# Kernel tuning notes

Hardware: AMD Instinct MI355X
Metric: run time of the kernel (lower is better)

## Reference

```python
import jax, jax.numpy as jnp
import numpy as np

L, D, V, F4 = 12, 768, 50304, 3072
B, T = 4, 1024


def setup_inputs() -> dict:
    key = jax.random.key(0)
    ks = jax.random.split(key, 12)
    s = 0.02
    return {
        "idx": jax.random.randint(ks[0], (B, T), 0, V),
        "targets": jax.random.randint(ks[1], (B, T), 0, V),
        "wte": jax.random.normal(ks[2], (V, D), jnp.float32) * s,  # tied with lm_head
        "pos_embed": jax.random.normal(ks[3], (L, D), jnp.float32),  # per-block (1,1,D) learned pos embed
        "dyt_alpha": jnp.full((L, 3), 0.5, jnp.float32),  # dyt, dyt2, dyt3 alphas
        "dyt_w": jnp.ones((L, 3, D), jnp.float32),
        "dyt_b": jnp.zeros((L, 3, D), jnp.float32),
        "Wq": jax.random.normal(ks[4], (L, D, D), jnp.float32) * s,
        "Wk": jax.random.normal(ks[5], (L, D, D), jnp.float32) * s,
        "Wv": jax.random.normal(ks[6], (L, D, D), jnp.float32) * s,
        "Wp": jax.random.normal(ks[7], (L, D, D), jnp.float32) * s,
        "bp": jnp.zeros((L, D), jnp.float32),
        "We": jax.random.normal(ks[8], (L, F4, D), jnp.float32) * s,
        "be": jnp.zeros((L, F4), jnp.float32),
        "Wc": jax.random.normal(ks[9], (L, D, F4), jnp.float32) * s,
        "bc": jnp.zeros((L, D), jnp.float32),
    }


def _dyt(x, a, w, b):
    return jnp.tanh(a * x) * w + b


def _forward(idx, targets, wte, pos_embed, dyt_alpha, dyt_w, dyt_b,
             Wq, Wk, Wv, Wp, bp, We, be, Wc, bc):
    b, t = idx.shape
    x = wte[idx]  # (b,t,D)
    pos = jnp.arange(t)
    pbias = -jnp.abs(pos[None, :] - pos[:, None]).astype(x.dtype)  # (t,t) ALiBi-style bias
    scale = 1.0 / np.sqrt(D)  # note: source scales by sqrt(emb_dim), not head dim
    total_kl = jnp.asarray(0.0, x.dtype)
    for l in range(L):
        xl = x + pos_embed[l][None, None, :]
        prior = _dyt(xl, dyt_alpha[l, 2], dyt_w[l, 2], dyt_b[l, 2])  # dyt3
        h = _dyt(xl, dyt_alpha[l, 0], dyt_w[l, 0], dyt_b[l, 0])      # dyt (dropout=0)
        Q = jnp.einsum('btd,od->bto', h, Wq[l])
        K = jnp.einsum('btd,od->bto', h, Wk[l])
        Vv = jnp.einsum('btd,od->bto', h, Wv[l])
        scores = jnp.einsum('btd,bsd->bts', Q, K) * scale + pbias  # (b,t,t), no causal mask
        aw = jax.nn.softmax(scores, axis=-1)
        ao = jnp.einsum('bts,bsd->btd', aw, Vv)
        ao = jnp.einsum('btd,od->bto', ao, Wp[l]) + bp[l]
        h2 = _dyt(ao, dyt_alpha[l, 1], dyt_w[l, 1], dyt_b[l, 1])     # dyt2
        h2 = jax.nn.gelu(jnp.einsum('btd,fd->btf', h2, We[l]) + be[l], approximate=False)
        h2 = jnp.einsum('btf,df->btd', h2, Wc[l]) + bc[l]
        posterior = h2 + prior
        m = 0.5 * (prior + posterior)
        lm = jax.nn.log_softmax(m, axis=-1)
        mp = jnp.exp(lm)
        lp = jax.nn.log_softmax(prior, axis=-1)
        lq = jax.nn.log_softmax(posterior, axis=-1)
        # F.kl_div(log_p, q, reduction='batchmean') = sum(q*(log q - log_p)) / batch
        kl = 0.5 * (jnp.sum(mp * (lm - lp)) + jnp.sum(mp * (lm - lq))) / b
        total_kl = total_kl + kl
        x = posterior
    logits = jnp.einsum('btd,vd->btv', x[:, -1:, :], wte)  # (b,1,V)
    full_logits = jnp.einsum('btd,vd->btv', x, wte)
    lsm = jax.nn.log_softmax(full_logits, axis=-1)
    nll = -jnp.take_along_axis(lsm, targets[..., None], axis=-1).squeeze(-1)
    loss = jnp.mean(nll) + total_kl * 0.1
    return logits, loss


def reference(idx, targets, wte, pos_embed, dyt_alpha, dyt_w, dyt_b,
              Wq, Wk, Wv, Wp, bp, We, be, Wc, bc):
    return _forward(idx, targets, wte, pos_embed, dyt_alpha, dyt_w, dyt_b,
                    Wq, Wk, Wv, Wp, bp, We, be, Wc, bc)
```

## Files before the change

### kernel.cpp

```cpp
#include <hip/hip_runtime.h>
#include <hip/hip_bf16.h>

typedef __attribute__((ext_vector_type(8))) short bf16x8;
typedef __attribute__((ext_vector_type(4))) float f32x4;

__device__ __forceinline__ short f2bf(float f) {
  unsigned u = __float_as_uint(f);
  u = u + 0x7fffu + ((u >> 16) & 1u);
  return (short)(u >> 16);
}
__device__ __forceinline__ float bf2f(short s) {
  return __uint_as_float(((unsigned)(unsigned short)s) << 16);
}

#define GLOB_CAST(p) ((const __attribute__((address_space(1))) void*)(p))
#define LDS_CAST(p) ((__attribute__((address_space(3))) void*)(p))
#define GLL16(g, l) __builtin_amdgcn_global_load_lds(GLOB_CAST(g), LDS_CAST(l), 16, 0, 0)

constexpr int EP_BF16 = 0, EP_SCORES = 1, EP_DYT = 2, EP_GELU = 3, EP_PRIOR = 4;

__global__ __launch_bounds__(256) void cvt_k(const float* __restrict__ src,
                                             short* __restrict__ dst, long n4) {
  const long s = (long)blockIdx.x * 256 + threadIdx.x;
  if (s >= n4) return;
  float4 v = ((const float4*)src)[s];
  short4 o = {f2bf(v.x), f2bf(v.y), f2bf(v.z), f2bf(v.w)};
  ((short4*)dst)[s] = o;
}

__global__ __launch_bounds__(256) void cvt_layer_k(
    const float* __restrict__ wq, const float* __restrict__ wk,
    const float* __restrict__ wv, const float* __restrict__ wp,
    const float* __restrict__ we, const float* __restrict__ wc,
    short* __restrict__ dst) {
  const long s = (long)blockIdx.x * 256 + threadIdx.x;
  const long e = s * 4;
  const float* src; long off;
  if (e < 589824)        { src = wq; off = e; }
  else if (e < 1179648)  { src = wk; off = e - 589824; }
  else if (e < 1769472)  { src = wv; off = e - 1179648; }
  else if (e < 2359296)  { src = wp; off = e - 1769472; }
  else if (e < 4718592)  { src = we; off = e - 2359296; }
  else                   { src = wc; off = e - 4718592; }
  float4 v = *(const float4*)(src + off);
  short4 o = {f2bf(v.x), f2bf(v.y), f2bf(v.z), f2bf(v.w)};
  *(short4*)(dst + e) = o;
}

__global__ __launch_bounds__(256) void embed_head_k(
    const int* __restrict__ idx, const float* __restrict__ wte,
    const float* __restrict__ pos, const float* __restrict__ alp,
    const float* __restrict__ w, const float* __restrict__ b,
    float* __restrict__ x, float* __restrict__ prior, short* __restrict__ h) {
  const long s = (long)blockIdx.x * 256 + threadIdx.x;
  const long row = s / 192;
  const int c4 = (int)(s % 192);
  float4 xv = ((const float4*)(wte + (long)idx[row] * 768))[c4];
  ((float4*)x)[s] = xv;
  float4 pv = ((const float4*)pos)[c4];
  float4 w0 = ((const float4*)w)[c4];
  float4 b0 = ((const float4*)b)[c4];
  float4 w2 = ((const float4*)(w + 1536))[c4];
  float4 b2 = ((const float4*)(b + 1536))[c4];
  const float a0 = alp[0], a2 = alp[2];
  float4 xl = {xv.x + pv.x, xv.y + pv.y, xv.z + pv.z, xv.w + pv.w};
  float4 pr = {tanhf(a2 * xl.x) * w2.x + b2.x, tanhf(a2 * xl.y) * w2.y + b2.y,
               tanhf(a2 * xl.z) * w2.z + b2.z, tanhf(a2 * xl.w) * w2.w + b2.w};
  ((float4*)prior)[s] = pr;
  short4 hh = {f2bf(tanhf(a0 * xl.x) * w0.x + b0.x),
               f2bf(tanhf(a0 * xl.y) * w0.y + b0.y),
               f2bf(tanhf(a0 * xl.z) * w0.z + b0.z),
               f2bf(tanhf(a0 * xl.w) * w0.w + b0.w)};
  ((short4*)h)[s] = hh;
}

template <int EP, int TN>
__global__ __launch_bounds__(256, 2) void gemm_bt(
    const short* __restrict__ A, const short* __restrict__ B,
    void* __restrict__ Cv, int K, int lda, int ldb, int ldc,
    long sA, long sB, long sC,
    const float* __restrict__ bias, const float* __restrict__ dw,
    const float* __restrict__ db, const float* __restrict__ alp,
    const float* __restrict__ prior, float scale) {
  constexpr int NF = TN / 32;
  __shared__ short As[128 * 64];
  __shared__ short Bs[TN * 64];
  const int tid = threadIdx.x, lane = tid & 63;
  const int wr = tid >> 7, wc = (tid >> 6) & 1;
  const long rowBase = (long)blockIdx.y * 128;
  const long colBase = (long)blockIdx.x * TN;
  const short* Ab = A + (long)blockIdx.z * sA;
  const short* Bb = B + (long)blockIdx.z * sB;
  const int srow = tid >> 3, sseg = tid & 7;
  const int ssegS = sseg ^ (srow & 7);

  f32x4 acc[4][NF];
#pragma unroll
  for (int m = 0; m < 4; ++m)
#pragma unroll
    for (int n = 0; n < NF; ++n) acc[m][n] = (f32x4){0.f, 0.f, 0.f, 0.f};

  const int q = lane >> 4, cl = lane & 15;
  const int rsw = cl & 7;

  for (int kt = 0; kt < K; kt += 64) {
#pragma unroll
    for (int i = 0; i < 4; ++i)
      GLL16(Ab + (rowBase + i * 32 + srow) * (long)lda + kt + ssegS * 8,
            As + ((i * 32 + srow) * 64 + sseg * 8));
#pragma unroll
    for (int i = 0; i < TN / 32; ++i)
      GLL16(Bb + (colBase + i * 32 + srow) * (long)ldb + kt + ssegS * 8,
            Bs + ((i * 32 + srow) * 64 + sseg * 8));
    __syncthreads();
#pragma unroll
    for (int kk = 0; kk < 2; ++kk) {
      const int sw = ((kk * 4 + q) ^ rsw) << 3;
      bf16x8 af[4], bfr[NF];
#pragma unroll
      for (int m = 0; m < 4; ++m)
        af[m] = *(const bf16x8*)&As[(wr * 64 + m * 16 + cl) * 64 + sw];
#pragma unroll
      for (int n = 0; n < NF; ++n)
        bfr[n] = *(const bf16x8*)&Bs[(wc * (TN / 2) + n * 16 + cl) * 64 + sw];
#pragma unroll
      for (int m = 0; m < 4; ++m)
#pragma unroll
        for (int n = 0; n < NF; ++n)
          acc[m][n] = __builtin_amdgcn_mfma_f32_16x16x32_bf16(af[m], bfr[n], acc[m][n], 0, 0, 0);
    }
    __syncthreads();
  }

#pragma unroll
  for (int m = 0; m < 4; ++m) {
#pragma unroll
    for (int n = 0; n < NF; ++n) {
#pragma unroll
      for (int j = 0; j < 4; ++j) {
        long r = rowBase + wr * 64 + m * 16 + q * 4 + j;
        long c = colBase + wc * (TN / 2) + n * 16 + cl;
        float v = acc[m][n][j];
        if constexpr (EP == EP_SCORES) {
          float pb = -fabsf((float)(int)(r - c));
          ((float*)Cv)[(long)blockIdx.z * sC + r * ldc + c] = v * scale + pb;
        } else if constexpr (EP == EP_BF16) {
          ((short*)Cv)[(long)blockIdx.z * sC + r * ldc + c] = f2bf(v);
        } else if constexpr (EP == EP_DYT) {
          float xv = v + bias[c];
          ((short*)Cv)[r * (long)ldc + c] = f2bf(tanhf(alp[0] * xv) * dw[c] + db[c]);
        } else if constexpr (EP == EP_GELU) {
          float xv = v + bias[c];
          ((short*)Cv)[r * (long)ldc + c] = f2bf(0.5f * xv * (1.f + erff(xv * 0.70710678118654752f)));
        } else if constexpr (EP == EP_PRIOR) {
          ((float*)Cv)[r * (long)ldc + c] = v + bias[c] + prior[r * (long)ldc + c];
        }
      }
    }
  }
}

__global__ __launch_bounds__(256) void transp_k(const short* __restrict__ V,
                                                short* __restrict__ Vt, int ldv) {
  __shared__ short t[32][33];
  const int b = blockIdx.z;
  const int d0 = blockIdx.x * 32, t0 = blockIdx.y * 32;
  const int tx = threadIdx.x & 31, ty = threadIdx.x >> 5;
  const short* Vb = V + (long)b * 1024 * ldv;
  short* Tb = Vt + (long)b * 768 * 1024;
#pragma unroll
  for (int i = 0; i < 4; ++i)
    t[ty + i * 8][tx] = Vb[(long)(t0 + ty + i * 8) * ldv + d0 + tx];
  __syncthreads();
#pragma unroll
  for (int i = 0; i < 4; ++i)
    Tb[(long)(d0 + ty + i * 8) * 1024 + t0 + tx] = t[tx][ty + i * 8];
}

__global__ __launch_bounds__(256) void softmax_k(float* __restrict__ sc) {
  const int lane = threadIdx.x & 63;
  const long row = (long)blockIdx.x * 4 + (threadIdx.x >> 6);
  const float4* p = (const float4*)(sc + row * 1024);
  float4 v[4];
  float mx = -3e38f;
#pragma unroll
  for (int i = 0; i < 4; ++i) {
    v[i] = p[lane * 4 + i];
    mx = fmaxf(mx, fmaxf(fmaxf(v[i].x, v[i].y), fmaxf(v[i].z, v[i].w)));
  }
#pragma unroll
  for (int o = 1; o < 64; o <<= 1) mx = fmaxf(mx, __shfl_xor(mx, o));
  float e[16];
  float s = 0.f;
#pragma unroll
  for (int i = 0; i < 4; ++i) {
    e[i * 4 + 0] = __expf(v[i].x - mx);
    e[i * 4 + 1] = __expf(v[i].y - mx);
    e[i * 4 + 2] = __expf(v[i].z - mx);
    e[i * 4 + 3] = __expf(v[i].w - mx);
    s += e[i * 4] + e[i * 4 + 1] + e[i * 4 + 2] + e[i * 4 + 3];
  }
#pragma unroll
  for (int o = 1; o < 64; o <<= 1) s += __shfl_xor(s, o);
  const float inv = 1.f / s;
  short4* dst = (short4*)((short*)sc + row * 2048);
#pragma unroll
  for (int i = 0; i < 4; ++i) {
    short4 o4 = {f2bf(e[i * 4] * inv), f2bf(e[i * 4 + 1] * inv),
                 f2bf(e[i * 4 + 2] * inv), f2bf(e[i * 4 + 3] * inv)};
    dst[lane * 4 + i] = o4;
  }
}

__global__ __launch_bounds__(256) void tail_k(
    float* __restrict__ prior, const float* __restrict__ post,
    const float* __restrict__ pos_n, const float* __restrict__ alp_n,
    const float* __restrict__ w_n, const float* __restrict__ b_n,
    short* __restrict__ h, short* __restrict__ xbf,
    double* __restrict__ acc, int last) {
  const int lane = threadIdx.x & 63;
  const long row = (long)blockIdx.x * 4 + (threadIdx.x >> 6);
  float* pp = prior + row * 768;
  const float* qq = post + row * 768;
  float p[12], q[12];
#pragma unroll
  for (int i = 0; i < 12; ++i) { p[i] = pp[lane + i * 64]; q[i] = qq[lane + i * 64]; }
  float mp = -3e38f, mq = -3e38f, mm = -3e38f;
#pragma unroll
  for (int i = 0; i < 12; ++i) {
    float m = 0.5f * (p[i] + q[i]);
    mp = fmaxf(mp, p[i]); mq = fmaxf(mq, q[i]); mm = fmaxf(mm, m);
  }
#pragma unroll
  for (int o = 1; o < 64; o <<= 1) {
    mp = fmaxf(mp, __shfl_xor(mp, o));
    mq = fmaxf(mq, __shfl_xor(mq, o));
    mm = fmaxf(mm, __shfl_xor(mm, o));
  }
  float sp = 0.f, sq = 0.f, sm = 0.f;
#pragma unroll
  for (int i = 0; i < 12; ++i) {
    sp += __expf(p[i] - mp);
    sq += __expf(q[i] - mq);
    sm += __expf(0.5f * (p[i] + q[i]) - mm);
  }
#pragma unroll
  for (int o = 1; o < 64; o <<= 1) {
    sp += __shfl_xor(sp, o); sq += __shfl_xor(sq, o); sm += __shfl_xor(sm, o);
  }
  const float lseP = mp + logf(sp), lseQ = mq + logf(sq), lseM = mm + logf(sm);
  float kl = 0.f;
#pragma unroll
  for (int i = 0; i < 12; ++i) {
    float m = 0.5f * (p[i] + q[i]);
    float lm = m - lseM;
    kl += __expf(lm) * (2.f * lm - (p[i] - lseP) - (q[i] - lseQ));
  }
#pragma unroll
  for (int o = 1; o < 64; o <<= 1) kl += __shfl_xor(kl, o);
  if (lane == 0) atomicAdd(&acc[0], (double)kl);

  if (last) {
#pragma unroll
    for (int i = 0; i < 12; ++i) xbf[row * 768 + lane + i * 64] = f2bf(q[i]);
  } else {
    const float a0 = alp_n[0], a2 = alp_n[2];
#pragma unroll
    for (int i = 0; i < 12; ++i) {
      const int col = lane + i * 64;
      float xl = q[i] + pos_n[col];
      pp[col] = tanhf(a2 * xl) * w_n[1536 + col] + b_n[1536 + col];
      h[row * 768 + col] = f2bf(tanhf(a0 * xl) * w_n[col] + b_n[col]);
    }
  }
}

__global__ __launch_bounds__(256, 2) void lse_gemm_k(
    const short* __restrict__ Xb, const short* __restrict__ Wt,
    float* __restrict__ pm, float* __restrict__ ps,
    float* __restrict__ logits_out, int G) {
  __shared__ short As[128 * 64];
  __shared__ short Bs[128 * 64];
  __shared__ float pmx[2][128], psm[2][128], rm[128], rs[128];
  const int tid = threadIdx.x, lane = tid & 63;
  const int wr = tid >> 7, wc = (tid >> 6) & 1;
  const int g = blockIdx.x;
  const long rowBase = (long)blockIdx.y * 128;
  const int srow = tid >> 3, sseg = tid & 7;
  const int ssegS = sseg ^ (srow & 7);
  const int q = lane >> 4, cl = lane & 15;
  const int rsw = cl & 7;
  if (tid < 128) { rm[tid] = -3e38f; rs[tid] = 0.f; }

  for (int tile = g; tile < 393; tile += G) {
    const long colBase = (long)tile * 128;
    f32x4 acc[4][4];
#pragma unroll
    for (int m = 0; m < 4; ++m)
#pragma unroll
      for (int n = 0; n < 4; ++n) acc[m][n] = (f32x4){0.f, 0.f, 0.f, 0.f};

    for (int kt = 0; kt < 768; kt += 64) {
#pragma unroll
      for (int i = 0; i < 4; ++i) {
        GLL16(Xb + (rowBase + i * 32 + srow) * 768L + kt + ssegS * 8,
              As + ((i * 32 + srow) * 64 + sseg * 8));
        GLL16(Wt + (colBase + i * 32 + srow) * 768L + kt + ssegS * 8,
              Bs + ((i * 32 + srow) * 64 + sseg * 8));
      }
      __syncthreads();
#pragma unroll
      for (int kk = 0; kk < 2; ++kk) {
        const int sw = ((kk * 4 + q) ^ rsw) << 3;
        bf16x8 af[4], bfr[4];
#pragma unroll
        for (int m = 0; m < 4; ++m)
          af[m] = *(const bf16x8*)&As[(wr * 64 + m * 16 + cl) * 64 + sw];
#pragma unroll
        for (int n = 0; n < 4; ++n)
          bfr[n] = *(const bf16x8*)&Bs[(wc * 64 + n * 16 + cl) * 64 + sw];
#pragma unroll
        for (int m = 0; m < 4; ++m)
#pragma unroll
          for (int n = 0; n < 4; ++n)
            acc[m][n] = __builtin_amdgcn_mfma_f32_16x16x32_bf16(af[m], bfr[n], acc[m][n], 0, 0, 0);
      }
      __syncthreads();
    }

#pragma unroll
    for (int m = 0; m < 4; ++m)
#pragma unroll
      for (int n = 0; n < 4; ++n)
#pragma unroll
        for (int j = 0; j < 4; ++j) {
          long r = rowBase + wr * 64 + m * 16 + q * 4 + j;
          if ((r & 1023) == 1023) {
            long c = colBase + wc * 64 + n * 16 + cl;
            logits_out[(r >> 10) * 50304 + c] = acc[m][n][j];
          }
        }

#pragma unroll
    for (int m = 0; m < 4; ++m) {
#pragma unroll
      for (int j = 0; j < 4; ++j) {
        float mx = acc[m][0][j];
#pragma unroll
        for (int n = 1; n < 4; ++n) mx = fmaxf(mx, acc[m][n][j]);
#pragma unroll
        for (int o = 1; o < 16; o <<= 1) mx = fmaxf(mx, __shfl_xor(mx, o));
        float sm = 0.f;
#pragma unroll
        for (int n = 0; n < 4; ++n) sm += __expf(acc[m][n][j] - mx);
#pragma unroll
        for (int o = 1; o < 16; o <<= 1) sm += __shfl_xor(sm, o);
        if (cl == 0) {
          int lr = wr * 64 + m * 16 + q * 4 + j;
          pmx[wc][lr] = mx;
          psm[wc][lr] = sm;
        }
      }
    }
    __syncthreads();
    if (tid < 128) {
      float m0 = pmx[0][tid], m1 = pmx[1][tid];
      float m2 = fmaxf(m0, m1);
      float s2 = psm[0][tid] * __expf(m0 - m2) + psm[1][tid] * __expf(m1 - m2);
      float mo = rm[tid], mn = fmaxf(mo, m2);
      rs[tid] = rs[tid] * __expf(mo - mn) + s2 * __expf(m2 - mn);
      rm[tid] = mn;
    }
    __syncthreads();
  }
  if (tid < 128) {
    long row = rowBase + tid;
    pm[row * G + g] = rm[tid];
    ps[row * G + g] = rs[tid];
  }
}

__global__ __launch_bounds__(256) void tlog_k(const short* __restrict__ xbf,
                                              const short* __restrict__ wtebf,
                                              const int* __restrict__ targets,
                                              float* __restrict__ tlog) {
  const int lane = threadIdx.x & 63;
  const long row = (long)blockIdx.x * 4 + (threadIdx.x >> 6);
  const long tgt = targets[row];
  const short* a = xbf + row * 768;
  const short* b = wtebf + tgt * 768;
  float s = 0.f;
#pragma unroll
  for (int i = 0; i < 12; ++i) s += bf2f(a[lane + i * 64]) * bf2f(b[lane + i * 64]);
#pragma unroll
  for (int o = 1; o < 64; o <<= 1) s += __shfl_xor(s, o);
  if (lane == 0) tlog[row] = s;
}

__global__ __launch_bounds__(256) void stage2_k(const float* __restrict__ pm,
                                                const float* __restrict__ ps,
                                                const float* __restrict__ tlog,
                                                double* __restrict__ acc, int G) {
  const long row = (long)blockIdx.x * 256 + threadIdx.x;
  float M = -3e38f;
  for (int gi = 0; gi < G; ++gi) M = fmaxf(M, pm[row * G + gi]);
  float S = 0.f;
  for (int gi = 0; gi < G; ++gi) S += ps[row * G + gi] * __expf(pm[row * G + gi] - M);
  float nll = (M + logf(S)) - tlog[row];
#pragma unroll
  for (int o = 1; o < 64; o <<= 1) nll += __shfl_xor(nll, o);
  if ((threadIdx.x & 63) == 0) atomicAdd(&acc[1], (double)nll);
}

__global__ void finalize_k(const double* __restrict__ acc, float* __restrict__ out) {
  if (threadIdx.x == 0)
    out[201216] = (float)(acc[1] / 4096.0 + 0.1 * 0.5 * acc[0] / 4.0);
}

constexpr size_t OFF_WTEBF = 0;
constexpr size_t OFF_LW    = 77266944;
constexpr size_t OFF_X     = 91422720;
constexpr size_t OFF_PRIOR = 104005632;
constexpr size_t OFF_HB    = 116588544;
constexpr size_t OFF_U1    = 122880000;
constexpr size_t OFF_QKV   = OFF_U1;
constexpr size_t OFF_VT    = OFF_U1 + 18874368;
constexpr size_t OFF_E     = OFF_U1;
constexpr size_t OFF_SC    = 148045824;
constexpr size_t OFF_AO    = 164823040;
constexpr size_t OFF_XBF   = 171114496;
constexpr size_t OFF_PM    = 177405952;
constexpr size_t OFF_PS    = 177799168;
constexpr size_t OFF_TLOG  = 178192384;
constexpr size_t OFF_ACC   = 178208768;
constexpr size_t WS_NEED   = 178208784;

extern "C" void kernel_launch(void* const* d_in, const int* in_sizes, int n_in,
                              void* d_out, int out_size, void* d_ws, size_t ws_size,
                              hipStream_t stream) {
  const int* idx = (const int*)d_in[0];
  const int* targets = (const int*)d_in[1];
  const float* wte = (const float*)d_in[2];
  const float* pos = (const float*)d_in[3];
  const float* dalpha = (const float*)d_in[4];
  const float* dytw = (const float*)d_in[5];
  const float* dytb = (const float*)d_in[6];
  const float* Wq = (const float*)d_in[7];
  const float* Wk = (const float*)d_in[8];
  const float* Wv = (const float*)d_in[9];
  const float* Wp = (const float*)d_in[10];
  const float* bp = (const float*)d_in[11];
  const float* We = (const float*)d_in[12];
  const float* be = (const float*)d_in[13];
  const float* Wc = (const float*)d_in[14];
  const float* bc = (const float*)d_in[15];
  float* out = (float*)d_out;

  if (ws_size < WS_NEED) return;
  char* ws = (char*)d_ws;
  short* WTEBF = (short*)(ws + OFF_WTEBF);
  short* LW = (short*)(ws + OFF_LW);
  float* X = (float*)(ws + OFF_X);
  float* PRIOR = (float*)(ws + OFF_PRIOR);
  short* HB = (short*)(ws + OFF_HB);
  short* QKVB = (short*)(ws + OFF_QKV);
  short* VT = (short*)(ws + OFF_VT);
  short* E = (short*)(ws + OFF_E);
  float* SC = (float*)(ws + OFF_SC);
  short* AW = (short*)(ws + OFF_SC);
  short* AO = (short*)(ws + OFF_AO);
  short* XBF = (short*)(ws + OFF_XBF);
  float* PM = (float*)(ws + OFF_PM);
  float* PS = (float*)(ws + OFF_PS);
  float* TLOG = (float*)(ws + OFF_TLOG);
  double* ACC = (double*)(ws + OFF_ACC);

  hipMemsetAsync(ACC, 0, 16, stream);
  cvt_k<<<37728, 256, 0, stream>>>(wte, WTEBF, 9658368);
  embed_head_k<<<3072, 256, 0, stream>>>(idx, wte, pos, dalpha, dytw, dytb, X, PRIOR, HB);

  const float scale = 0.03608439182435161f;

  for (int l = 0; l < 12; ++l) {
    cvt_layer_k<<<6912, 256, 0, stream>>>(Wq + (long)l * 589824, Wk + (long)l * 589824,
                                          Wv + (long)l * 589824, Wp + (long)l * 589824,
                                          We + (long)l * 2359296, Wc + (long)l * 2359296, LW);
    gemm_bt<EP_BF16, 128><<<dim3(18, 32, 1), 256, 0, stream>>>(
        HB, LW, QKVB, 768, 768, 768, 2304, 0, 0, 0,
        nullptr, nullptr, nullptr, nullptr, nullptr, 0.f);
    transp_k<<<dim3(24, 32, 4), 256, 0, stream>>>(QKVB + 1536, VT, 2304);
    gemm_bt<EP_SCORES, 64><<<dim3(16, 8, 4), 256, 0, stream>>>(
        QKVB, QKVB + 768, SC, 768, 2304, 2304, 1024,
        2359296, 2359296, 1048576, nullptr, nullptr, nullptr, nullptr, nullptr, scale);
    softmax_k<<<1024, 256, 0, stream>>>(SC);
    gemm_bt<EP_BF16, 64><<<dim3(12, 8, 4), 256, 0, stream>>>(
        AW, VT, AO, 1024, 2048, 1024, 768, 2097152, 786432, 786432,
        nullptr, nullptr, nullptr, nullptr, nullptr, 0.f);
    gemm_bt<EP_DYT, 64><<<dim3(12, 32, 1), 256, 0, stream>>>(
        AO, LW + 1769472, HB, 768, 768, 768, 768, 0, 0, 0,
        bp + l * 768, dytw + l * 2304 + 768, dytb + l * 2304 + 768,
        dalpha + l * 3 + 1, nullptr, 0.f);
    gemm_bt<EP_GELU, 128><<<dim3(24, 32, 1), 256, 0, stream>>>(
        HB, LW + 2359296, E, 768, 768, 768, 3072, 0, 0, 0,
        be + l * 3072, nullptr, nullptr, nullptr, nullptr, 0.f);
    gemm_bt<EP_PRIOR, 64><<<dim3(12, 32, 1), 256, 0, stream>>>(
        E, LW + 4718592, X, 3072, 3072, 3072, 768, 0, 0, 0,
        bc + l * 768, nullptr, nullptr, nullptr, PRIOR, 0.f);
    tail_k<<<1024, 256, 0, stream>>>(PRIOR, X, pos + (l + 1) * 768,
                                     dalpha + (l + 1) * 3, dytw + (l + 1) * 2304,
                                     dytb + (l + 1) * 2304, HB, XBF, ACC, l == 11);
  }

  lse_gemm_k<<<dim3(24, 32), 256, 0, stream>>>(XBF, WTEBF, PM, PS, out, 24);
  tlog_k<<<1024, 256, 0, stream>>>(XBF, WTEBF, targets, TLOG);
  stage2_k<<<16, 256, 0, stream>>>(PM, PS, TLOG, ACC, 24);
  finalize_k<<<1, 64, 0, stream>>>(ACC, out);
}
```

Baseline: 3.111 ms.

## Fuse V transpose into QKV GEMM, batch weight conversion, add BK template

The QKV GEMM gains an epilogue that writes V directly in transposed layout, which removes the separate transpose kernel. When the workspace is large enough, all layer weights are converted to bf16 in one kernel up front instead of once per layer. The GEMM also gets a K-tile template parameter, set to 128 for the narrow-N GEMMs so they need fewer sync iterations, at the cost of more LDS per block. The transposed V stores are uncoalesced and the big path depends on the workspace size the harness provides.

```diff
diff --git a/kernel.cpp b/kernel.cpp
--- a/kernel.cpp
+++ b/kernel.cpp
@@ -17,7 +17,7 @@
 #define LDS_CAST(p) ((__attribute__((address_space(3))) void*)(p))
 #define GLL16(g, l) __builtin_amdgcn_global_load_lds(GLOB_CAST(g), LDS_CAST(l), 16, 0, 0)
 
-constexpr int EP_BF16 = 0, EP_SCORES = 1, EP_DYT = 2, EP_GELU = 3, EP_PRIOR = 4;
+constexpr int EP_BF16 = 0, EP_SCORES = 1, EP_DYT = 2, EP_GELU = 3, EP_PRIOR = 4, EP_QKVT = 5;
 
 __global__ __launch_bounds__(256) void cvt_k(const float* __restrict__ src,
                                              short* __restrict__ dst, long n4) {
@@ -45,6 +45,27 @@
   float4 v = *(const float4*)(src + off);
   short4 o = {f2bf(v.x), f2bf(v.y), f2bf(v.z), f2bf(v.w)};
   *(short4*)(dst + e) = o;
+}
+
+__global__ __launch_bounds__(256) void cvt_all_k(
+    const float* __restrict__ wq, const float* __restrict__ wk,
+    const float* __restrict__ wv, const float* __restrict__ wp,
+    const float* __restrict__ we, const float* __restrict__ wc,
+    short* __restrict__ dst) {
+  const long s = (long)blockIdx.x * 256 + threadIdx.x;
+  if (s >= 21233664L) return;
+  const long l = s / 1769472;
+  const long e = (s - l * 1769472) * 4;
+  const float* src; long off;
+  if (e < 589824)        { src = wq + l * 589824;  off = e; }
+  else if (e < 1179648)  { src = wk + l * 589824;  off = e - 589824; }
+  else if (e < 1769472)  { src = wv + l * 589824;  off = e - 1179648; }
+  else if (e < 2359296)  { src = wp + l * 589824;  off = e - 1769472; }
+  else if (e < 4718592)  { src = we + l * 2359296; off = e - 2359296; }
+  else                   { src = wc + l * 2359296; off = e - 4718592; }
+  float4 v = *(const float4*)(src + off);
+  short4 o = {f2bf(v.x), f2bf(v.y), f2bf(v.z), f2bf(v.w)};
+  *(short4*)(dst + l * 7077888 + e) = o;
 }
 
 __global__ __launch_bounds__(256) void embed_head_k(
@@ -74,24 +95,27 @@
   ((short4*)h)[s] = hh;
 }
 
-template <int EP, int TN>
+template <int EP, int TN, int BK>
 __global__ __launch_bounds__(256, 2) void gemm_bt(
     const short* __restrict__ A, const short* __restrict__ B,
-    void* __restrict__ Cv, int K, int lda, int ldb, int ldc,
+    void* __restrict__ Cv, short* __restrict__ vt,
+    int K, int lda, int ldb, int ldc,
     long sA, long sB, long sC,
     const float* __restrict__ bias, const float* __restrict__ dw,
     const float* __restrict__ db, const float* __restrict__ alp,
     const float* __restrict__ prior, float scale) {
   constexpr int NF = TN / 32;
-  __shared__ short As[128 * 64];
-  __shared__ short Bs[TN * 64];
+  constexpr int SEGS = BK / 8;
+  constexpr int RPR = 2048 / BK;
+  __shared__ short As[128 * BK];
+  __shared__ short Bs[TN * BK];
   const int tid = threadIdx.x, lane = tid & 63;
   const int wr = tid >> 7, wc = (tid >> 6) & 1;
   const long rowBase = (long)blockIdx.y * 128;
   const long colBase = (long)blockIdx.x * TN;
   const short* Ab = A + (long)blockIdx.z * sA;
   const short* Bb = B + (long)blockIdx.z * sB;
-  const int srow = tid >> 3, sseg = tid & 7;
+  const int srow = tid / SEGS, sseg = tid % SEGS;
   const int ssegS = sseg ^ (srow & 7);
 
   f32x4 acc[4][NF];
@@ -103,26 +127,30 @@
   const int q = lane >> 4, cl = lane & 15;
   const int rsw = cl & 7;
 
-  for (int kt = 0; kt < K; kt += 64) {
-#pragma unroll
-    for (int i = 0; i < 4; ++i)
-      GLL16(Ab + (rowBase + i * 32 + srow) * (long)lda + kt + ssegS * 8,
-            As + ((i * 32 + srow) * 64 + sseg * 8));
-#pragma unroll
-    for (int i = 0; i < TN / 32; ++i)
-      GLL16(Bb + (colBase + i * 32 + srow) * (long)ldb + kt + ssegS * 8,
-            Bs + ((i * 32 + srow) * 64 + sseg * 8));
+  for (int kt = 0; kt < K; kt += BK) {
+#pragma unroll
+    for (int i = 0; i < BK / 16; ++i) {
+      const int row = i * RPR + srow;
+      GLL16(Ab + (rowBase + row) * (long)lda + kt + ssegS * 8,
+            As + (row * BK + sseg * 8));
+    }
+#pragma unroll
+    for (int i = 0; i < TN * BK / 2048; ++i) {
+      const int row = i * RPR + srow;
+      GLL16(Bb + (colBase + row) * (long)ldb + kt + ssegS * 8,
+            Bs + (row * BK + sseg * 8));
+    }
     __syncthreads();
 #pragma unroll
-    for (int kk = 0; kk < 2; ++kk) {
+    for (int kk = 0; kk < BK / 32; ++kk) {
       const int sw = ((kk * 4 + q) ^ rsw) << 3;
       bf16x8 af[4], bfr[NF];
 #pragma unroll
       for (int m = 0; m < 4; ++m)
-        af[m] = *(const bf16x8*)&As[(wr * 64 + m * 16 + cl) * 64 + sw];
+        af[m] = *(const bf16x8*)&As[(wr * 64 + m * 16 + cl) * BK + sw];
 #pragma unroll
       for (int n = 0; n < NF; ++n)
-        bfr[n] = *(const bf16x8*)&Bs[(wc * (TN / 2) + n * 16 + cl) * 64 + sw];
+        bfr[n] = *(const bf16x8*)&Bs[(wc * (TN / 2) + n * 16 + cl) * BK + sw];
 #pragma unroll
       for (int m = 0; m < 4; ++m)
 #pragma unroll
@@ -146,6 +174,11 @@
           ((float*)Cv)[(long)blockIdx.z * sC + r * ldc + c] = v * scale + pb;
         } else if constexpr (EP == EP_BF16) {
           ((short*)Cv)[(long)blockIdx.z * sC + r * ldc + c] = f2bf(v);
+        } else if constexpr (EP == EP_QKVT) {
+          if (c < 1536)
+            ((short*)Cv)[r * (long)ldc + c] = f2bf(v);
+          else
+            vt[(r >> 10) * 786432 + (c - 1536) * 1024 + (r & 1023)] = f2bf(v);
         } else if constexpr (EP == EP_DYT) {
           float xv = v + bias[c];
           ((short*)Cv)[r * (long)ldc + c] = f2bf(tanhf(alp[0] * xv) * dw[c] + db[c]);
@@ -158,23 +191,6 @@
       }
     }
   }
-}
-
-__global__ __launch_bounds__(256) void transp_k(const short* __restrict__ V,
-                                                short* __restrict__ Vt, int ldv) {
-  __shared__ short t[32][33];
-  const int b = blockIdx.z;
-  const int d0 = blockIdx.x * 32, t0 = blockIdx.y * 32;
-  const int tx = threadIdx.x & 31, ty = threadIdx.x >> 5;
-  const short* Vb = V + (long)b * 1024 * ldv;
-  short* Tb = Vt + (long)b * 768 * 1024;
-#pragma unroll
-  for (int i = 0; i < 4; ++i)
-    t[ty + i * 8][tx] = Vb[(long)(t0 + ty + i * 8) * ldv + d0 + tx];
-  __syncthreads();
-#pragma unroll
-  for (int i = 0; i < 4; ++i)
-    Tb[(long)(d0 + ty + i * 8) * 1024 + t0 + tx] = t[tx][ty + i * 8];
 }
 
 __global__ __launch_bounds__(256) void softmax_k(float* __restrict__ sc) {
@@ -433,7 +449,9 @@
 constexpr size_t OFF_PS    = 177799168;
 constexpr size_t OFF_TLOG  = 178192384;
 constexpr size_t OFF_ACC   = 178208768;
-constexpr size_t WS_NEED   = 178208784;
+constexpr size_t WS_SMALL  = 178208784;
+constexpr size_t OFF_LWALL = 178208784;
+constexpr size_t WS_BIG    = 348078096;
 
 extern "C" void kernel_launch(void* const* d_in, const int* in_sizes, int n_in,
                               void* d_out, int out_size, void* d_ws, size_t ws_size,
@@ -456,10 +474,12 @@
   const float* bc = (const float*)d_in[15];
   float* out = (float*)d_out;
 
-  if (ws_size < WS_NEED) return;
+  if (ws_size < WS_SMALL) return;
+  const bool big = ws_size >= WS_BIG;
   char* ws = (char*)d_ws;
   short* WTEBF = (short*)(ws + OFF_WTEBF);
   short* LW = (short*)(ws + OFF_LW);
+  short* LWALL = (short*)(ws + OFF_LWALL);
   float* X = (float*)(ws + OFF_X);
   float* PRIOR = (float*)(ws + OFF_PRIOR);
   short* HB = (short*)(ws + OFF_HB);
@@ -477,34 +497,41 @@
 
   hipMemsetAsync(ACC, 0, 16, stream);
   cvt_k<<<37728, 256, 0, stream>>>(wte, WTEBF, 9658368);
+  if (big)
+    cvt_all_k<<<82944, 256, 0, stream>>>(Wq, Wk, Wv, Wp, We, Wc, LWALL);
   embed_head_k<<<3072, 256, 0, stream>>>(idx, wte, pos, dalpha, dytw, dytb, X, PRIOR, HB);
 
   const float scale = 0.03608439182435161f;
 
   for (int l = 0; l < 12; ++l) {
-    cvt_layer_k<<<6912, 256, 0, stream>>>(Wq + (long)l * 589824, Wk + (long)l * 589824,
-                                          Wv + (long)l * 589824, Wp + (long)l * 589824,
-                                          We + (long)l * 2359296, Wc + (long)l * 2359296, LW);
-    gemm_bt<EP_BF16, 128><<<dim3(18, 32, 1), 256, 0, stream>>>(
-        HB, LW, QKVB, 768, 768, 768, 2304, 0, 0, 0,
+    const short* lw;
+    if (big) {
+      lw = LWALL + (long)l * 7077888;
+    } else {
+      cvt_layer_k<<<6912, 256, 0, stream>>>(Wq + (long)l * 589824, Wk + (long)l * 589824,
+                                            Wv + (long)l * 589824, Wp + (long)l * 589824,
+                                            We + (long)l * 2359296, Wc + (long)l * 2359296, LW);
+      lw = LW;
+    }
+    gemm_bt<EP_QKVT, 128, 64><<<dim3(18, 32, 1), 256, 0, stream>>>(
+        HB, lw, QKVB, VT, 768, 768, 768, 2304, 0, 0, 0,
         nullptr, nullptr, nullptr, nullptr, nullptr, 0.f);
-    transp_k<<<dim3(24, 32, 4), 256, 0, stream>>>(QKVB + 1536, VT, 2304);
-    gemm_bt<EP_SCORES, 64><<<dim3(16, 8, 4), 256, 0, stream>>>(
-        QKVB, QKVB + 768, SC, 768, 2304, 2304, 1024,
+    gemm_bt<EP_SCORES, 64, 128><<<dim3(16, 8, 4), 256, 0, stream>>>(
+        QKVB, QKVB + 768, SC, nullptr, 768, 2304, 2304, 1024,
         2359296, 2359296, 1048576, nullptr, nullptr, nullptr, nullptr, nullptr, scale);
     softmax_k<<<1024, 256, 0, stream>>>(SC);
-    gemm_bt<EP_BF16, 64><<<dim3(12, 8, 4), 256, 0, stream>>>(
-        AW, VT, AO, 1024, 2048, 1024, 768, 2097152, 786432, 786432,
+    gemm_bt<EP_BF16, 64, 128><<<dim3(12, 8, 4), 256, 0, stream>>>(
+        AW, VT, AO, nullptr, 1024, 2048, 1024, 768, 2097152, 786432, 786432,
         nullptr, nullptr, nullptr, nullptr, nullptr, 0.f);
-    gemm_bt<EP_DYT, 64><<<dim3(12, 32, 1), 256, 0, stream>>>(
-        AO, LW + 1769472, HB, 768, 768, 768, 768, 0, 0, 0,
+    gemm_bt<EP_DYT, 64, 128><<<dim3(12, 32, 1), 256, 0, stream>>>(
+        AO, lw + 1769472, HB, nullptr, 768, 768, 768, 768, 0, 0, 0,
         bp + l * 768, dytw + l * 2304 + 768, dytb + l * 2304 + 768,
         dalpha + l * 3 + 1, nullptr, 0.f);
-    gemm_bt<EP_GELU, 128><<<dim3(24, 32, 1), 256, 0, stream>>>(
-        HB, LW + 2359296, E, 768, 768, 768, 3072, 0, 0, 0,
+    gemm_bt<EP_GELU, 128, 64><<<dim3(24, 32, 1), 256, 0, stream>>>(
+        HB, lw + 2359296, E, nullptr, 768, 768, 768, 3072, 0, 0, 0,
         be + l * 3072, nullptr, nullptr, nullptr, nullptr, 0.f);
-    gemm_bt<EP_PRIOR, 64><<<dim3(12, 32, 1), 256, 0, stream>>>(
-        E, LW + 4718592, X, 3072, 3072, 3072, 768, 0, 0, 0,
+    gemm_bt<EP_PRIOR, 64, 128><<<dim3(12, 32, 1), 256, 0, stream>>>(
+        E, lw + 4718592, X, nullptr, 3072, 3072, 3072, 768, 0, 0, 0,
         bc + l * 768, nullptr, nullptr, nullptr, PRIOR, 0.f);
     tail_k<<<1024, 256, 0, stream>>>(PRIOR, X, pos + (l + 1) * 768,
                                      dalpha + (l + 1) * 3, dytw + (l + 1) * 2304,
```

Result: slower. 3.280 ms (+5.5%).

## Store bf16 scores with bias in softmax, batch weight conversion, remap LSE blocks per XCD

Applied to the files above, without the earlier changes.

Three independent changes. The scores GEMM now writes bf16 scores without the ALiBi bias, and the softmax adds the bias itself and works in place on bf16, which halves score traffic. When the workspace is large enough, all layer weights are converted to bf16 in one up-front kernel instead of one per-layer launch. The LSE GEMM block index is remapped so that blocks sharing a vocab tile group land on the same XCD. Rounding scores to bf16 before softmax adds precision loss, and the big-workspace path runs only if the harness provides enough workspace.

```diff
diff --git a/kernel.cpp b/kernel.cpp
--- a/kernel.cpp
+++ b/kernel.cpp
@@ -45,6 +45,27 @@
   float4 v = *(const float4*)(src + off);
   short4 o = {f2bf(v.x), f2bf(v.y), f2bf(v.z), f2bf(v.w)};
   *(short4*)(dst + e) = o;
+}
+
+__global__ __launch_bounds__(256) void cvt_all_k(
+    const float* __restrict__ wq, const float* __restrict__ wk,
+    const float* __restrict__ wv, const float* __restrict__ wp,
+    const float* __restrict__ we, const float* __restrict__ wc,
+    short* __restrict__ dst) {
+  const long s = (long)blockIdx.x * 256 + threadIdx.x;
+  if (s >= 21233664L) return;
+  const long l = s / 1769472;
+  const long e = (s - l * 1769472) * 4;
+  const float* src; long off;
+  if (e < 589824)        { src = wq + l * 589824;  off = e; }
+  else if (e < 1179648)  { src = wk + l * 589824;  off = e - 589824; }
+  else if (e < 1769472)  { src = wv + l * 589824;  off = e - 1179648; }
+  else if (e < 2359296)  { src = wp + l * 589824;  off = e - 1769472; }
+  else if (e < 4718592)  { src = we + l * 2359296; off = e - 2359296; }
+  else                   { src = wc + l * 2359296; off = e - 4718592; }
+  float4 v = *(const float4*)(src + off);
+  short4 o = {f2bf(v.x), f2bf(v.y), f2bf(v.z), f2bf(v.w)};
+  *(short4*)(dst + l * 7077888 + e) = o;
 }
 
 __global__ __launch_bounds__(256) void embed_head_k(
@@ -142,8 +163,7 @@
         long c = colBase + wc * (TN / 2) + n * 16 + cl;
         float v = acc[m][n][j];
         if constexpr (EP == EP_SCORES) {
-          float pb = -fabsf((float)(int)(r - c));
-          ((float*)Cv)[(long)blockIdx.z * sC + r * ldc + c] = v * scale + pb;
+          ((short*)Cv)[(long)blockIdx.z * sC + r * ldc + c] = f2bf(v * scale);
         } else if constexpr (EP == EP_BF16) {
           ((short*)Cv)[(long)blockIdx.z * sC + r * ldc + c] = f2bf(v);
         } else if constexpr (EP == EP_DYT) {
@@ -177,39 +197,40 @@
     Tb[(long)(d0 + ty + i * 8) * 1024 + t0 + tx] = t[tx][ty + i * 8];
 }
 
-__global__ __launch_bounds__(256) void softmax_k(float* __restrict__ sc) {
+__global__ __launch_bounds__(256) void softmax_k(short* __restrict__ sc) {
   const int lane = threadIdx.x & 63;
   const long row = (long)blockIdx.x * 4 + (threadIdx.x >> 6);
-  const float4* p = (const float4*)(sc + row * 1024);
-  float4 v[4];
+  const int t = (int)(row & 1023);
+  short* p = sc + row * 1024;
+  const int c0 = lane * 16;
+  bf16x8 a = *(const bf16x8*)(p + c0);
+  bf16x8 b = *(const bf16x8*)(p + c0 + 8);
+  float v[16];
   float mx = -3e38f;
 #pragma unroll
-  for (int i = 0; i < 4; ++i) {
-    v[i] = p[lane * 4 + i];
-    mx = fmaxf(mx, fmaxf(fmaxf(v[i].x, v[i].y), fmaxf(v[i].z, v[i].w)));
-  }
+  for (int i = 0; i < 8; ++i) {
+    v[i] = bf2f(a[i]) - fabsf((float)(t - (c0 + i)));
+    v[i + 8] = bf2f(b[i]) - fabsf((float)(t - (c0 + 8 + i)));
+  }
+#pragma unroll
+  for (int i = 0; i < 16; ++i) mx = fmaxf(mx, v[i]);
 #pragma unroll
   for (int o = 1; o < 64; o <<= 1) mx = fmaxf(mx, __shfl_xor(mx, o));
   float e[16];
   float s = 0.f;
 #pragma unroll
-  for (int i = 0; i < 4; ++i) {
-    e[i * 4 + 0] = __expf(v[i].x - mx);
-    e[i * 4 + 1] = __expf(v[i].y - mx);
-    e[i * 4 + 2] = __expf(v[i].z - mx);
-    e[i * 4 + 3] = __expf(v[i].w - mx);
-    s += e[i * 4] + e[i * 4 + 1] + e[i * 4 + 2] + e[i * 4 + 3];
-  }
+  for (int i = 0; i < 16; ++i) { e[i] = __expf(v[i] - mx); s += e[i]; }
 #pragma unroll
   for (int o = 1; o < 64; o <<= 1) s += __shfl_xor(s, o);
   const float inv = 1.f / s;
-  short4* dst = (short4*)((short*)sc + row * 2048);
-#pragma unroll
-  for (int i = 0; i < 4; ++i) {
-    short4 o4 = {f2bf(e[i * 4] * inv), f2bf(e[i * 4 + 1] * inv),
-                 f2bf(e[i * 4 + 2] * inv), f2bf(e[i * 4 + 3] * inv)};
-    dst[lane * 4 + i] = o4;
-  }
+  bf16x8 o0, o1;
+#pragma unroll
+  for (int i = 0; i < 8; ++i) {
+    o0[i] = f2bf(e[i] * inv);
+    o1[i] = f2bf(e[i + 8] * inv);
+  }
+  *(bf16x8*)(p + c0) = o0;
+  *(bf16x8*)(p + c0 + 8) = o1;
 }
 
 __global__ __launch_bounds__(256) void tail_k(
@@ -278,21 +299,25 @@
 __global__ __launch_bounds__(256, 2) void lse_gemm_k(
     const short* __restrict__ Xb, const short* __restrict__ Wt,
     float* __restrict__ pm, float* __restrict__ ps,
-    float* __restrict__ logits_out, int G) {
+    float* __restrict__ logits_out) {
   __shared__ short As[128 * 64];
   __shared__ short Bs[128 * 64];
   __shared__ float pmx[2][128], psm[2][128], rm[128], rs[128];
   const int tid = threadIdx.x, lane = tid & 63;
   const int wr = tid >> 7, wc = (tid >> 6) & 1;
-  const int g = blockIdx.x;
-  const long rowBase = (long)blockIdx.y * 128;
+  const int id = blockIdx.y * 24 + blockIdx.x;
+  const int xcd = id & 7;
+  const int kk_ = id >> 3;
+  const int g = xcd * 3 + (kk_ >> 5);
+  const int y = kk_ & 31;
+  const long rowBase = (long)y * 128;
   const int srow = tid >> 3, sseg = tid & 7;
   const int ssegS = sseg ^ (srow & 7);
   const int q = lane >> 4, cl = lane & 15;
   const int rsw = cl & 7;
   if (tid < 128) { rm[tid] = -3e38f; rs[tid] = 0.f; }
 
-  for (int tile = g; tile < 393; tile += G) {
+  for (int tile = g; tile < 393; tile += 24) {
     const long colBase = (long)tile * 128;
     f32x4 acc[4][4];
 #pragma unroll
@@ -375,8 +400,8 @@
   }
   if (tid < 128) {
     long row = rowBase + tid;
-    pm[row * G + g] = rm[tid];
-    ps[row * G + g] = rs[tid];
+    pm[row * 24 + g] = rm[tid];
+    ps[row * 24 + g] = rs[tid];
   }
 }
 
@@ -433,7 +458,9 @@
 constexpr size_t OFF_PS    = 177799168;
 constexpr size_t OFF_TLOG  = 178192384;
 constexpr size_t OFF_ACC   = 178208768;
-constexpr size_t WS_NEED   = 178208784;
+constexpr size_t WS_SMALL  = 178208784;
+constexpr size_t OFF_LWALL = 178208784;
+constexpr size_t WS_BIG    = 348078096;
 
 extern "C" void kernel_launch(void* const* d_in, const int* in_sizes, int n_in,
                               void* d_out, int out_size, void* d_ws, size_t ws_size,
@@ -456,18 +483,19 @@
   const float* bc = (const float*)d_in[15];
   float* out = (float*)d_out;
 
-  if (ws_size < WS_NEED) return;
+  if (ws_size < WS_SMALL) return;
+  const bool big = ws_size >= WS_BIG;
   char* ws = (char*)d_ws;
   short* WTEBF = (short*)(ws + OFF_WTEBF);
   short* LW = (short*)(ws + OFF_LW);
+  short* LWALL = (short*)(ws + OFF_LWALL);
   float* X = (float*)(ws + OFF_X);
   float* PRIOR = (float*)(ws + OFF_PRIOR);
   short* HB = (short*)(ws + OFF_HB);
   short* QKVB = (short*)(ws + OFF_QKV);
   short* VT = (short*)(ws + OFF_VT);
   short* E = (short*)(ws + OFF_E);
-  float* SC = (float*)(ws + OFF_SC);
-  short* AW = (short*)(ws + OFF_SC);
+  short* SC = (short*)(ws + OFF_SC);
   short* AO = (short*)(ws + OFF_AO);
   short* XBF = (short*)(ws + OFF_XBF);
   float* PM = (float*)(ws + OFF_PM);
@@ -477,16 +505,24 @@
 
   hipMemsetAsync(ACC, 0, 16, stream);
   cvt_k<<<37728, 256, 0, stream>>>(wte, WTEBF, 9658368);
+  if (big)
+    cvt_all_k<<<82944, 256, 0, stream>>>(Wq, Wk, Wv, Wp, We, Wc, LWALL);
   embed_head_k<<<3072, 256, 0, stream>>>(idx, wte, pos, dalpha, dytw, dytb, X, PRIOR, HB);
 
   const float scale = 0.03608439182435161f;
 
   for (int l = 0; l < 12; ++l) {
-    cvt_layer_k<<<6912, 256, 0, stream>>>(Wq + (long)l * 589824, Wk + (long)l * 589824,
-                                          Wv + (long)l * 589824, Wp + (long)l * 589824,
-                                          We + (long)l * 2359296, Wc + (long)l * 2359296, LW);
+    const short* lw;
+    if (big) {
+      lw = LWALL + (long)l * 7077888;
+    } else {
+      cvt_layer_k<<<6912, 256, 0, stream>>>(Wq + (long)l * 589824, Wk + (long)l * 589824,
+                                            Wv + (long)l * 589824, Wp + (long)l * 589824,
+                                            We + (long)l * 2359296, Wc + (long)l * 2359296, LW);
+      lw = LW;
+    }
     gemm_bt<EP_BF16, 128><<<dim3(18, 32, 1), 256, 0, stream>>>(
-        HB, LW, QKVB, 768, 768, 768, 2304, 0, 0, 0,
+        HB, lw, QKVB, 768, 768, 768, 2304, 0, 0, 0,
         nullptr, nullptr, nullptr, nullptr, nullptr, 0.f);
     transp_k<<<dim3(24, 32, 4), 256, 0, stream>>>(QKVB + 1536, VT, 2304);
     gemm_bt<EP_SCORES, 64><<<dim3(16, 8, 4), 256, 0, stream>>>(
@@ -494,24 +530,24 @@
         2359296, 2359296, 1048576, nullptr, nullptr, nullptr, nullptr, nullptr, scale);
     softmax_k<<<1024, 256, 0, stream>>>(SC);
     gemm_bt<EP_BF16, 64><<<dim3(12, 8, 4), 256, 0, stream>>>(
-        AW, VT, AO, 1024, 2048, 1024, 768, 2097152, 786432, 786432,
+        SC, VT, AO, 1024, 1024, 1024, 768, 1048576, 786432, 786432,
         nullptr, nullptr, nullptr, nullptr, nullptr, 0.f);
     gemm_bt<EP_DYT, 64><<<dim3(12, 32, 1), 256, 0, stream>>>(
-        AO, LW + 1769472, HB, 768, 768, 768, 768, 0, 0, 0,
+        AO, lw + 1769472, HB, 768, 768, 768, 768, 0, 0, 0,
         bp + l * 768, dytw + l * 2304 + 768, dytb + l * 2304 + 768,
         dalpha + l * 3 + 1, nullptr, 0.f);
     gemm_bt<EP_GELU, 128><<<dim3(24, 32, 1), 256, 0, stream>>>(
-        HB, LW + 2359296, E, 768, 768, 768, 3072, 0, 0, 0,
+        HB, lw + 2359296, E, 768, 768, 768, 3072, 0, 0, 0,
         be + l * 3072, nullptr, nullptr, nullptr, nullptr, 0.f);
     gemm_bt<EP_PRIOR, 64><<<dim3(12, 32, 1), 256, 0, stream>>>(
-        E, LW + 4718592, X, 3072, 3072, 3072, 768, 0, 0, 0,
+        E, lw + 4718592, X, 3072, 3072, 3072, 768, 0, 0, 0,
         bc + l * 768, nullptr, nullptr, nullptr, PRIOR, 0.f);
     tail_k<<<1024, 256, 0, stream>>>(PRIOR, X, pos + (l + 1) * 768,
                                      dalpha + (l + 1) * 3, dytw + (l + 1) * 2304,
                                      dytb + (l + 1) * 2304, HB, XBF, ACC, l == 11);
   }
 
-  lse_gemm_k<<<dim3(24, 32), 256, 0, stream>>>(XBF, WTEBF, PM, PS, out, 24);
+  lse_gemm_k<<<dim3(24, 32), 256, 0, stream>>>(XBF, WTEBF, PM, PS, out);
   tlog_k<<<1024, 256, 0, stream>>>(XBF, WTEBF, targets, TLOG);
   stage2_k<<<16, 256, 0, stream>>>(PM, PS, TLOG, ACC, 24);
   finalize_k<<<1, 64, 0, stream>>>(ACC, out);
```

New measurement: 3.349 ms. 7.6% more time.
